# Kernel tuning notes

Measured on AMD Instinct MI355X. Metric: run time of the kernel, lower is better.

## Reference

```python
import jax, jax.numpy as jnp
import numpy as np

B, S, D, H = 2, 2048, 1024, 16
DK = D // H  # 64


def setup_inputs() -> dict:
    key = jax.random.key(0)
    ks = jax.random.split(key, 9)
    w = lambda k_, shp: jax.random.normal(k_, shp, dtype=jnp.float32) * 0.02
    inp = {
        "q": jax.random.normal(ks[0], (B, S, D), dtype=jnp.float32),
        "k": jax.random.normal(ks[1], (B, S, D), dtype=jnp.float32),
        "v": jax.random.normal(ks[2], (B, S, D), dtype=jnp.float32),
        # causal mask, broadcastable over [B, H, S, S]; 0 -> masked
        "mask": jnp.tril(jnp.ones((S, S), dtype=jnp.int32))[None, None, :, :],
        "Wq": w(ks[3], (D, D)), "bq": w(ks[4], (D,)),
        "Wk": w(ks[5], (D, D)), "bk": w(ks[6], (D,)),
        "Wv": w(ks[7], (D, D)), "bv": w(ks[8], (D,)),
    }
    return inp


def _head_split(x):
    # [B, S, D] -> [B, H, S, DK]
    return x.reshape(B, S, H, DK).transpose(0, 2, 1, 3)


def reference(q, k, v, mask, Wq, bq, Wk, bk, Wv, bv):
    qh = _head_split(q @ Wq + bq)
    kh = _head_split(k @ Wk + bk)
    vh = _head_split(v @ Wv + bv)

    scores = jnp.einsum("bhqd,bhkd->bhqk", qh, kh) / jnp.sqrt(jnp.float32(DK))
    scores = jnp.where(mask == 0, -jnp.inf, scores)
    # original subtracts the GLOBAL max of the whole score tensor, then softmax
    scores = jax.nn.softmax(scores - jnp.max(scores), axis=-1)
    scores = jnp.where(jnp.isnan(scores), 0.0, scores)  # fully-masked rows -> 0

    out = jnp.einsum("bhqk,bhkd->bhqd", scores, vh)
    return out.transpose(0, 2, 1, 3).reshape(B, S, D)
```

## Files before the change

### kernel.cpp

```cpp
#include <hip/hip_runtime.h>
#include <hip/hip_bf16.h>
#include <stdint.h>

#define BB 2
#define SS 2048
#define DD 1024
#define HH 16
#define DKK 64

typedef __attribute__((ext_vector_type(8)))  __bf16 bfvec8;
typedef __attribute__((ext_vector_type(4)))  __bf16 bfvec4;
typedef __attribute__((ext_vector_type(4)))  float  f32x4;
typedef __attribute__((ext_vector_type(16))) float  f32x16;
typedef __attribute__((ext_vector_type(4)))  unsigned int u32x4;

__device__ __forceinline__ float exp2_fast(float x) {
    float r;
    asm("v_exp_f32 %0, %1" : "=v"(r) : "v"(x));
    return r;
}
__device__ __forceinline__ uint32_t cvt_pk(float lo, float hi) {
    uint32_t r;
    asm("v_cvt_pk_bf16_f32 %0, %1, %2" : "=v"(r) : "v"(lo), "v"(hi));
    return r;
}
__device__ __forceinline__ void plswap(uint32_t &x, uint32_t &y) {
    asm("v_permlane32_swap_b32 %0, %1" : "+v"(x), "+v"(y));
}
__device__ __forceinline__ f32x16 zero16() {
    return (f32x16){0.f,0.f,0.f,0.f,0.f,0.f,0.f,0.f,
                    0.f,0.f,0.f,0.f,0.f,0.f,0.f,0.f};
}
#define MFMA32(A, B, C) __builtin_amdgcn_mfma_f32_32x32x16_bf16((A), (B), (C), 0, 0, 0)

#define PACK(st, bofs, pa) do {                                   \
    uint32_t A1 = cvt_pk((st)[(bofs)+0], (st)[(bofs)+1]);         \
    uint32_t B1 = cvt_pk((st)[(bofs)+4], (st)[(bofs)+5]);         \
    uint32_t A2 = cvt_pk((st)[(bofs)+2], (st)[(bofs)+3]);         \
    uint32_t B2 = cvt_pk((st)[(bofs)+6], (st)[(bofs)+7]);         \
    plswap(A1, B1); plswap(A2, B2);                               \
    u32x4 u_; u_[0] = A1; u_[1] = A2; u_[2] = B1; u_[3] = B2;     \
    (pa) = __builtin_bit_cast(bfvec8, u_);                        \
} while (0)

__global__ void wt_kernel(const float* __restrict__ Wq, const float* __restrict__ Wk,
                          const float* __restrict__ Wv,
                          __bf16* __restrict__ Wtq, __bf16* __restrict__ Wtk,
                          __bf16* __restrict__ Wtv) {
    const float* W  = (blockIdx.z == 0) ? Wq  : (blockIdx.z == 1) ? Wk  : Wv;
    __bf16*      Wt = (blockIdx.z == 0) ? Wtq : (blockIdx.z == 1) ? Wtk : Wtv;
    __shared__ float tile[32][33];
    int k0 = blockIdx.x * 32;
    int n0 = blockIdx.y * 32;
    int tx = threadIdx.x, ty = threadIdx.y;
    for (int j = 0; j < 32; j += 8)
        tile[ty + j][tx] = W[(size_t)(k0 + ty + j) * DD + n0 + tx];
    __syncthreads();
    for (int j = 0; j < 32; j += 8)
        Wt[(size_t)(n0 + ty + j) * DD + k0 + tx] = (__bf16)tile[tx][ty + j];
}

#define BM 128
#define BN 128
#define BKP 64
#define LDA 72
#define LDV 68

__global__ __launch_bounds__(256)
void proj_kernel(const float* __restrict__ Xq, const float* __restrict__ Xk,
                 const float* __restrict__ Xv,
                 const __bf16* __restrict__ Wtq, const __bf16* __restrict__ Wtk,
                 const __bf16* __restrict__ Wtv,
                 const float* __restrict__ bq, const float* __restrict__ bk,
                 const float* __restrict__ bv,
                 __bf16* __restrict__ Qh, __bf16* __restrict__ Kh,
                 __bf16* __restrict__ VtG)
{
    int z = blockIdx.z;
    const float*  X    = (z == 0) ? Xq  : (z == 1) ? Xk  : Xv;
    const __bf16* Wt   = (z == 0) ? Wtq : (z == 1) ? Wtk : Wtv;
    const float*  bias = (z == 0) ? bq  : (z == 1) ? bk  : bv;
    const float scale  = (z == 0) ? 0.125f * 1.44269504088896340736f : 1.0f;

    __shared__ __align__(16) char praw[2 * BM * LDA * 2];
    __bf16* As = reinterpret_cast<__bf16*>(praw);
    __bf16* Bs = reinterpret_cast<__bf16*>(praw + BM * LDA * 2);

    int row_tile = blockIdx.x * 4 + (blockIdx.y >> 3);
    int col_tile = blockIdx.y & 7;
    int row0 = row_tile * BM;
    int col0 = col_tile * BN;

    int t    = threadIdx.x;
    int lane = t & 63;
    int w    = t >> 6;
    int wm   = w >> 1, wn = w & 1;
    int l15  = lane & 15;
    int hi   = lane >> 4;
    int kg   = hi * 8;

    f32x4 acc[4][4];
    for (int i = 0; i < 4; ++i)
        for (int j = 0; j < 4; ++j)
            acc[i][j] = (f32x4){0.f, 0.f, 0.f, 0.f};

    int rr = t >> 3;
    int c8 = (t & 7) * 8;

    f32x4 a0[4], a1[4];
    bfvec8 br[4];
    for (int i = 0; i < 4; ++i) {
        int row = rr + 32 * i;
        const float* xp = &X[(size_t)(row0 + row) * DD + c8];
        a0[i] = *reinterpret_cast<const f32x4*>(xp);
        a1[i] = *reinterpret_cast<const f32x4*>(xp + 4);
        br[i] = *reinterpret_cast<const bfvec8*>(
            &Wt[(size_t)(col0 + row) * DD + c8]);
    }

    #pragma unroll 2
    for (int k0 = 0; k0 < DD; k0 += BKP) {
        for (int i = 0; i < 4; ++i) {
            int row = rr + 32 * i;
            bfvec8 av;
            av[0] = (__bf16)a0[i][0]; av[1] = (__bf16)a0[i][1];
            av[2] = (__bf16)a0[i][2]; av[3] = (__bf16)a0[i][3];
            av[4] = (__bf16)a1[i][0]; av[5] = (__bf16)a1[i][1];
            av[6] = (__bf16)a1[i][2]; av[7] = (__bf16)a1[i][3];
            *reinterpret_cast<bfvec8*>(&As[row * LDA + c8]) = av;
            *reinterpret_cast<bfvec8*>(&Bs[row * LDA + c8]) = br[i];
        }
        __syncthreads();

        bool more = (k0 + BKP) < DD;
        if (more) {
            int kn = k0 + BKP;
            for (int i = 0; i < 4; ++i) {
                int row = rr + 32 * i;
                const float* xp = &X[(size_t)(row0 + row) * DD + kn + c8];
                a0[i] = *reinterpret_cast<const f32x4*>(xp);
                a1[i] = *reinterpret_cast<const f32x4*>(xp + 4);
                br[i] = *reinterpret_cast<const bfvec8*>(
                    &Wt[(size_t)(col0 + row) * DD + kn + c8]);
            }
        }

        __builtin_amdgcn_s_setprio(1);
        for (int kk = 0; kk < BKP; kk += 32) {
            bfvec8 af[4], bf[4];
            for (int fm = 0; fm < 4; ++fm)
                af[fm] = *reinterpret_cast<const bfvec8*>(
                    &As[(wm * 64 + fm * 16 + l15) * LDA + kk + kg]);
            for (int fn = 0; fn < 4; ++fn)
                bf[fn] = *reinterpret_cast<const bfvec8*>(
                    &Bs[(wn * 64 + fn * 16 + l15) * LDA + kk + kg]);
            for (int fm = 0; fm < 4; ++fm)
                for (int fn = 0; fn < 4; ++fn)
                    acc[fm][fn] = __builtin_amdgcn_mfma_f32_16x16x32_bf16(
                        af[fm], bf[fn], acc[fm][fn], 0, 0, 0);
        }
        __builtin_amdgcn_s_setprio(0);
        __syncthreads();
    }

    if (z != 2) {
        __bf16* Out = (z == 0) ? Qh : Kh;
        for (int fn = 0; fn < 4; ++fn) {
            int n  = col0 + wn * 64 + fn * 16 + l15;
            float bvl = bias[n];
            int h = n >> 6, dk = n & 63;
            for (int fm = 0; fm < 4; ++fm) {
                int mbase = row0 + wm * 64 + fm * 16 + hi * 4;
                for (int r = 0; r < 4; ++r) {
                    int m = mbase + r;
                    int b = m >> 11, s = m & 2047;
                    float v = (acc[fm][fn][r] + bvl) * scale;
                    Out[(((size_t)(b * HH + h) * SS) + s) * DKK + dk] = (__bf16)v;
                }
            }
        }
    } else {
        __bf16* tw = reinterpret_cast<__bf16*>(praw + w * (64 * LDV * 2));
        for (int fn = 0; fn < 4; ++fn) {
            int n  = col0 + wn * 64 + fn * 16 + l15;
            float bvl = bias[n];
            for (int fm = 0; fm < 4; ++fm) {
                int sl = fm * 16 + hi * 4;
                for (int r = 0; r < 4; ++r)
                    tw[(sl + r) * LDV + fn * 16 + l15] =
                        (__bf16)(acc[fm][fn][r] + bvl);
            }
        }
        int h  = (col0 + wn * 64) >> 6;
        int b  = row0 >> 11;
        int bh = b * HH + h;
        int sg = (row0 & 2047) + wm * 64;
        int d  = lane;
        __bf16* dst = VtG + ((size_t)bh * DKK + d) * SS + sg;
        for (int c = 0; c < 64; c += 8) {
            bfvec8 v;
            #pragma unroll
            for (int j = 0; j < 8; ++j)
                v[j] = tw[(c + j) * LDV + d];
            *reinterpret_cast<bfvec8*>(&dst[c]) = v;
        }
    }
}

#define QB 128
#define KB 64
#define LDK 72
#define NT (SS / QB)

__global__ __launch_bounds__(512, 4)
void attn_kernel(const __bf16* __restrict__ Qh, const __bf16* __restrict__ Kh,
                 const __bf16* __restrict__ VtG, float* __restrict__ out)
{
    __shared__ __align__(16) char ldsraw[36864 + 1024];
    __bf16* KsA = reinterpret_cast<__bf16*>(ldsraw);
    __bf16* KsB = reinterpret_cast<__bf16*>(ldsraw + 9216);
    __bf16* VsA = reinterpret_cast<__bf16*>(ldsraw + 18432);
    __bf16* VsB = reinterpret_cast<__bf16*>(ldsraw + 27648);
    float*  smc = reinterpret_cast<float*>(ldsraw + 36864);
    float*  mrg = reinterpret_cast<float*>(ldsraw);
    float*  ml  = reinterpret_cast<float*>(ldsraw + 32768);

    int bh = blockIdx.x;
    int qt = (NT - 1) - blockIdx.y;
    const size_t base = (size_t)bh * SS * DKK;
    const __bf16* Kb = Kh + base;
    const __bf16* Vb = VtG + base;

    int t    = threadIdx.x;
    int lane = t & 63;
    int w    = t >> 6;
    int rg   = w & 3;
    int half = w >> 2;
    int l31  = lane & 31;
    int hi2  = lane >> 5;

    int a    = qt * QB + rg * 32;
    int qrow = a + l31;

    const __bf16* ksb = half ? KsB : KsA;
    const __bf16* vsb = half ? VsB : VsA;

    bfvec8 qf0, qf1, qf2, qf3;
    {
        const __bf16* qp = &Qh[base + (size_t)qrow * DKK + hi2 * 8];
        qf0 = *reinterpret_cast<const bfvec8*>(qp);
        qf1 = *reinterpret_cast<const bfvec8*>(qp + 16);
        qf2 = *reinterpret_cast<const bfvec8*>(qp + 32);
        qf3 = *reinterpret_cast<const bfvec8*>(qp + 48);
    }

    f32x16 acc0 = zero16(), acc1 = zero16();
    float mrow = -1e30f, lrow = 0.f;

    int nkv   = (a + 31) / KB + 1;
    int pairs = qt + 1;

    int srow = t >> 3;
    int c8   = (t & 7) * 8;

    {
        bfvec8 ka = *reinterpret_cast<const bfvec8*>(&Kb[(size_t)srow * DKK + c8]);
        bfvec8 va = *reinterpret_cast<const bfvec8*>(&Vb[(size_t)srow * SS + c8]);
        bfvec8 kb = *reinterpret_cast<const bfvec8*>(&Kb[(size_t)(64 + srow) * DKK + c8]);
        bfvec8 vb = *reinterpret_cast<const bfvec8*>(&Vb[(size_t)srow * SS + 64 + c8]);
        *reinterpret_cast<bfvec8*>(&KsA[srow * LDK + c8]) = ka;
        *reinterpret_cast<bfvec8*>(&VsA[srow * LDK + c8]) = va;
        *reinterpret_cast<bfvec8*>(&KsB[srow * LDK + c8]) = kb;
        *reinterpret_cast<bfvec8*>(&VsB[srow * LDK + c8]) = vb;
    }
    __syncthreads();

    for (int j = 0; ; ++j) {
        bool more = (j + 1) < pairs;

        bfvec8 pkA, pvA, pkB, pvB;
        if (more) {
            int t0 = (2 * j + 2) * KB;
            pkA = *reinterpret_cast<const bfvec8*>(&Kb[(size_t)(t0 + srow) * DKK + c8]);
            pvA = *reinterpret_cast<const bfvec8*>(&Vb[(size_t)srow * SS + t0 + c8]);
            pkB = *reinterpret_cast<const bfvec8*>(&Kb[(size_t)(t0 + 64 + srow) * DKK + c8]);
            pvB = *reinterpret_cast<const bfvec8*>(&Vb[(size_t)srow * SS + t0 + 64 + c8]);
        }

        int tj = 2 * j + half;
        if (tj < nkv) {
            int kv64 = tj * KB;

            f32x16 st0 = zero16(), st1 = zero16();
            {
                int off = l31 * LDK + hi2 * 8;
                bfvec8 k0 = *reinterpret_cast<const bfvec8*>(&ksb[off]);
                bfvec8 k1 = *reinterpret_cast<const bfvec8*>(&ksb[off + 16]);
                bfvec8 k2 = *reinterpret_cast<const bfvec8*>(&ksb[off + 32]);
                bfvec8 k3 = *reinterpret_cast<const bfvec8*>(&ksb[off + 48]);
                st0 = MFMA32(k0, qf0, st0); st0 = MFMA32(k1, qf1, st0);
                st0 = MFMA32(k2, qf2, st0); st0 = MFMA32(k3, qf3, st0);
                int off1 = off + 32 * LDK;
                bfvec8 m0 = *reinterpret_cast<const bfvec8*>(&ksb[off1]);
                bfvec8 m1 = *reinterpret_cast<const bfvec8*>(&ksb[off1 + 16]);
                bfvec8 m2v = *reinterpret_cast<const bfvec8*>(&ksb[off1 + 32]);
                bfvec8 m3 = *reinterpret_cast<const bfvec8*>(&ksb[off1 + 48]);
                st1 = MFMA32(m0, qf0, st1); st1 = MFMA32(m1, qf1, st1);
                st1 = MFMA32(m2v, qf2, st1); st1 = MFMA32(m3, qf3, st1);
            }

            if (kv64 + 63 > a) {
                #pragma unroll
                for (int r = 0; r < 16; ++r) {
                    int cr = ((r & 3) + 8 * (r >> 2)) + 4 * hi2;
                    st0[r] = (kv64 + cr      > qrow) ? -1e30f : st0[r];
                    st1[r] = (kv64 + 32 + cr > qrow) ? -1e30f : st1[r];
                }
            }

            float m2 = -1e30f;
            #pragma unroll
            for (int r = 0; r < 16; ++r) {
                m2 = fmaxf(m2, st0[r]);
                m2 = fmaxf(m2, st1[r]);
            }
            m2 = fmaxf(m2, __shfl_xor(m2, 32));

            float corr = 1.0f;
            if (!__all(m2 - mrow <= 8.0f)) {
                float mn = fmaxf(mrow, m2);
                corr = exp2_fast(mrow - mn);
                mrow = mn;
                smc[w * 32 + l31] = corr;
                #pragma unroll
                for (int r = 0; r < 16; ++r) {
                    float rc = smc[w * 32 + ((r & 3) + 8 * (r >> 2)) + 4 * hi2];
                    acc0[r] *= rc;
                    acc1[r] *= rc;
                }
            }

            float rs = 0.f;
            #pragma unroll
            for (int r = 0; r < 16; ++r) {
                float p0 = exp2_fast(st0[r] - mrow); st0[r] = p0;
                float p1 = exp2_fast(st1[r] - mrow); st1[r] = p1;
                rs += p0 + p1;
            }
            rs += __shfl_xor(rs, 32);
            lrow = lrow * corr + rs;

            bfvec8 pa0, pa1, pa2, pa3;
            PACK(st0, 0, pa0); PACK(st0, 8, pa1);
            PACK(st1, 0, pa2); PACK(st1, 8, pa3);

            {
                int voff = l31 * LDK + hi2 * 8;
                bfvec8 v0 = *reinterpret_cast<const bfvec8*>(&vsb[voff]);
                bfvec8 v1 = *reinterpret_cast<const bfvec8*>(&vsb[voff + 16]);
                bfvec8 v2 = *reinterpret_cast<const bfvec8*>(&vsb[voff + 32]);
                bfvec8 v3 = *reinterpret_cast<const bfvec8*>(&vsb[voff + 48]);
                acc0 = MFMA32(pa0, v0, acc0); acc0 = MFMA32(pa1, v1, acc0);
                acc0 = MFMA32(pa2, v2, acc0); acc0 = MFMA32(pa3, v3, acc0);
                int voff1 = voff + 32 * LDK;
                bfvec8 u0 = *reinterpret_cast<const bfvec8*>(&vsb[voff1]);
                bfvec8 u1 = *reinterpret_cast<const bfvec8*>(&vsb[voff1 + 16]);
                bfvec8 u2 = *reinterpret_cast<const bfvec8*>(&vsb[voff1 + 32]);
                bfvec8 u3 = *reinterpret_cast<const bfvec8*>(&vsb[voff1 + 48]);
                acc1 = MFMA32(pa0, u0, acc1); acc1 = MFMA32(pa1, u1, acc1);
                acc1 = MFMA32(pa2, u2, acc1); acc1 = MFMA32(pa3, u3, acc1);
            }
        }

        if (!more) break;
        __syncthreads();
        *reinterpret_cast<bfvec8*>(&KsA[srow * LDK + c8]) = pkA;
        *reinterpret_cast<bfvec8*>(&VsA[srow * LDK + c8]) = pvA;
        *reinterpret_cast<bfvec8*>(&KsB[srow * LDK + c8]) = pkB;
        *reinterpret_cast<bfvec8*>(&VsB[srow * LDK + c8]) = pvB;
        __syncthreads();
    }

    __syncthreads();
    if (half == 1) {
        float* dst = mrg + ((size_t)(rg * 64 + lane)) * 32;
        #pragma unroll
        for (int r = 0; r < 16; ++r) { dst[r] = acc0[r]; dst[16 + r] = acc1[r]; }
        if (hi2 == 0) {
            ml[rg * 32 + l31]       = mrow;
            ml[128 + rg * 32 + l31] = lrow;
        }
    }
    __syncthreads();
    if (half == 0) {
        float mU = ml[rg * 32 + l31];
        float lU = ml[128 + rg * 32 + l31];
        float mS = fmaxf(mrow, mU);
        float cL = exp2_fast(mrow - mS), cU = exp2_fast(mU - mS);
        float li = 1.0f / (lrow * cL + lU * cU);
        smc[rg * 32 + l31]       = cL * li;
        smc[(rg + 4) * 32 + l31] = cU * li;
        const float* src = mrg + ((size_t)(rg * 64 + lane)) * 32;
        int b = bh >> 4, h = bh & 15;
        #pragma unroll
        for (int r = 0; r < 16; ++r) {
            int cr = ((r & 3) + 8 * (r >> 2)) + 4 * hi2;
            float sA = smc[rg * 32 + cr];
            float sB = smc[(rg + 4) * 32 + cr];
            int sg = a + cr;
            size_t o = ((size_t)(b * SS + sg)) * DD + h * DKK + l31;
            out[o]      = acc0[r] * sA + src[r]      * sB;
            out[o + 32] = acc1[r] * sA + src[16 + r] * sB;
        }
    }
}

extern "C" void kernel_launch(void* const* d_in, const int* in_sizes, int n_in,
                              void* d_out, int out_size, void* d_ws, size_t ws_size,
                              hipStream_t stream)
{
    const float* q  = (const float*)d_in[0];
    const float* k  = (const float*)d_in[1];
    const float* v  = (const float*)d_in[2];
    const float* Wq = (const float*)d_in[4];
    const float* bq = (const float*)d_in[5];
    const float* Wk = (const float*)d_in[6];
    const float* bk = (const float*)d_in[7];
    const float* Wv = (const float*)d_in[8];
    const float* bv = (const float*)d_in[9];
    float* out = (float*)d_out;

    char* ws = (char*)d_ws;
    __bf16* Qh  = (__bf16*)(ws + (size_t)0);
    __bf16* Kh  = (__bf16*)(ws + (size_t)8  * 1024 * 1024);
    __bf16* VtG = (__bf16*)(ws + (size_t)24 * 1024 * 1024);
    __bf16* Wtq = (__bf16*)(ws + (size_t)32 * 1024 * 1024);
    __bf16* Wtk = (__bf16*)(ws + (size_t)34 * 1024 * 1024);
    __bf16* Wtv = (__bf16*)(ws + (size_t)36 * 1024 * 1024);

    wt_kernel<<<dim3(32, 32, 3), dim3(32, 8), 0, stream>>>(
        Wq, Wk, Wv, Wtq, Wtk, Wtv);

    proj_kernel<<<dim3(8, 32, 3), 256, 0, stream>>>(
        q, k, v, Wtq, Wtk, Wtv, bq, bk, bv, Qh, Kh, VtG);

    attn_kernel<<<dim3(32, NT), 512, 0, stream>>>(Qh, Kh, VtG, out);
}
```

Measured before the change: 96.55 us.

## Pre-convert activations to bf16 and stage projection tiles with global_load_lds

Adds a separate kernel that converts the fp32 q/k/v activations to bf16, using the output buffer and a workspace slot as scratch. The projection GEMM then loads bf16 tiles straight into LDS through global_load_lds, which removes the register prefetch and in-register conversion. It also drops the LDS row padding, so the MFMA fragment reads may hit bank conflicts. The register double-buffer prefetch is gone, so global loads are no longer overlapped with compute, and the extra kernel adds a full read and write pass over the activations.

```diff
diff --git a/kernel.cpp b/kernel.cpp
--- a/kernel.cpp
+++ b/kernel.cpp
@@ -13,6 +13,13 @@
 typedef __attribute__((ext_vector_type(4)))  float  f32x4;
 typedef __attribute__((ext_vector_type(16))) float  f32x16;
 typedef __attribute__((ext_vector_type(4)))  unsigned int u32x4;
+
+typedef __attribute__((address_space(1))) const unsigned int gas_uint;
+typedef __attribute__((address_space(3))) unsigned int las_uint;
+
+__device__ __forceinline__ void gload16(const void* g, void* l) {
+    __builtin_amdgcn_global_load_lds((gas_uint*)g, (las_uint*)l, 16, 0, 0);
+}
 
 __device__ __forceinline__ float exp2_fast(float x) {
     float r;
@@ -42,6 +49,23 @@
     u32x4 u_; u_[0] = A1; u_[1] = A2; u_[2] = B1; u_[3] = B2;     \
     (pa) = __builtin_bit_cast(bfvec8, u_);                        \
 } while (0)
+
+__global__ void xcvt_kernel(const float* __restrict__ q, const float* __restrict__ k,
+                            const float* __restrict__ v,
+                            __bf16* __restrict__ xq, __bf16* __restrict__ xk,
+                            __bf16* __restrict__ xv) {
+    const float* src = (blockIdx.z == 0) ? q  : (blockIdx.z == 1) ? k  : v;
+    __bf16*      dst = (blockIdx.z == 0) ? xq : (blockIdx.z == 1) ? xk : xv;
+    size_t i = ((size_t)blockIdx.x * 256 + threadIdx.x) * 8;
+    f32x4 a = *reinterpret_cast<const f32x4*>(&src[i]);
+    f32x4 b = *reinterpret_cast<const f32x4*>(&src[i + 4]);
+    bfvec8 o;
+    o[0] = (__bf16)a[0]; o[1] = (__bf16)a[1];
+    o[2] = (__bf16)a[2]; o[3] = (__bf16)a[3];
+    o[4] = (__bf16)b[0]; o[5] = (__bf16)b[1];
+    o[6] = (__bf16)b[2]; o[7] = (__bf16)b[3];
+    *reinterpret_cast<bfvec8*>(&dst[i]) = o;
+}
 
 __global__ void wt_kernel(const float* __restrict__ Wq, const float* __restrict__ Wk,
                           const float* __restrict__ Wv,
@@ -63,12 +87,11 @@
 #define BM 128
 #define BN 128
 #define BKP 64
-#define LDA 72
 #define LDV 68
 
 __global__ __launch_bounds__(256)
-void proj_kernel(const float* __restrict__ Xq, const float* __restrict__ Xk,
-                 const float* __restrict__ Xv,
+void proj_kernel(const __bf16* __restrict__ Xq, const __bf16* __restrict__ Xk,
+                 const __bf16* __restrict__ Xv,
                  const __bf16* __restrict__ Wtq, const __bf16* __restrict__ Wtk,
                  const __bf16* __restrict__ Wtv,
                  const float* __restrict__ bq, const float* __restrict__ bk,
@@ -77,14 +100,14 @@
                  __bf16* __restrict__ VtG)
 {
     int z = blockIdx.z;
-    const float*  X    = (z == 0) ? Xq  : (z == 1) ? Xk  : Xv;
+    const __bf16* X    = (z == 0) ? Xq  : (z == 1) ? Xk  : Xv;
     const __bf16* Wt   = (z == 0) ? Wtq : (z == 1) ? Wtk : Wtv;
     const float*  bias = (z == 0) ? bq  : (z == 1) ? bk  : bv;
     const float scale  = (z == 0) ? 0.125f * 1.44269504088896340736f : 1.0f;
 
-    __shared__ __align__(16) char praw[2 * BM * LDA * 2];
+    __shared__ __align__(16) char praw[36864];
     __bf16* As = reinterpret_cast<__bf16*>(praw);
-    __bf16* Bs = reinterpret_cast<__bf16*>(praw + BM * LDA * 2);
+    __bf16* Bs = reinterpret_cast<__bf16*>(praw + 16384);
 
     int row_tile = blockIdx.x * 4 + (blockIdx.y >> 3);
     int col_tile = blockIdx.y & 7;
@@ -104,56 +127,28 @@
         for (int j = 0; j < 4; ++j)
             acc[i][j] = (f32x4){0.f, 0.f, 0.f, 0.f};
 
-    int rr = t >> 3;
-    int c8 = (t & 7) * 8;
-
-    f32x4 a0[4], a1[4];
-    bfvec8 br[4];
-    for (int i = 0; i < 4; ++i) {
-        int row = rr + 32 * i;
-        const float* xp = &X[(size_t)(row0 + row) * DD + c8];
-        a0[i] = *reinterpret_cast<const f32x4*>(xp);
-        a1[i] = *reinterpret_cast<const f32x4*>(xp + 4);
-        br[i] = *reinterpret_cast<const bfvec8*>(
-            &Wt[(size_t)(col0 + row) * DD + c8]);
-    }
+    int gr = lane >> 3;
+    int gc = (lane & 7) * 8;
 
     #pragma unroll 2
     for (int k0 = 0; k0 < DD; k0 += BKP) {
+        #pragma unroll
         for (int i = 0; i < 4; ++i) {
-            int row = rr + 32 * i;
-            bfvec8 av;
-            av[0] = (__bf16)a0[i][0]; av[1] = (__bf16)a0[i][1];
-            av[2] = (__bf16)a0[i][2]; av[3] = (__bf16)a0[i][3];
-            av[4] = (__bf16)a1[i][0]; av[5] = (__bf16)a1[i][1];
-            av[6] = (__bf16)a1[i][2]; av[7] = (__bf16)a1[i][3];
-            *reinterpret_cast<bfvec8*>(&As[row * LDA + c8]) = av;
-            *reinterpret_cast<bfvec8*>(&Bs[row * LDA + c8]) = br[i];
+            int r = w * 32 + i * 8;
+            gload16(&X [(size_t)(row0 + r + gr) * DD + k0 + gc], &As[r * BKP]);
+            gload16(&Wt[(size_t)(col0 + r + gr) * DD + k0 + gc], &Bs[r * BKP]);
         }
         __syncthreads();
-
-        bool more = (k0 + BKP) < DD;
-        if (more) {
-            int kn = k0 + BKP;
-            for (int i = 0; i < 4; ++i) {
-                int row = rr + 32 * i;
-                const float* xp = &X[(size_t)(row0 + row) * DD + kn + c8];
-                a0[i] = *reinterpret_cast<const f32x4*>(xp);
-                a1[i] = *reinterpret_cast<const f32x4*>(xp + 4);
-                br[i] = *reinterpret_cast<const bfvec8*>(
-                    &Wt[(size_t)(col0 + row) * DD + kn + c8]);
-            }
-        }
 
         __builtin_amdgcn_s_setprio(1);
         for (int kk = 0; kk < BKP; kk += 32) {
             bfvec8 af[4], bf[4];
             for (int fm = 0; fm < 4; ++fm)
                 af[fm] = *reinterpret_cast<const bfvec8*>(
-                    &As[(wm * 64 + fm * 16 + l15) * LDA + kk + kg]);
+                    &As[(wm * 64 + fm * 16 + l15) * BKP + kk + kg]);
             for (int fn = 0; fn < 4; ++fn)
                 bf[fn] = *reinterpret_cast<const bfvec8*>(
-                    &Bs[(wn * 64 + fn * 16 + l15) * LDA + kk + kg]);
+                    &Bs[(wn * 64 + fn * 16 + l15) * BKP + kk + kg]);
             for (int fm = 0; fm < 4; ++fm)
                 for (int fn = 0; fn < 4; ++fn)
                     acc[fm][fn] = __builtin_amdgcn_mfma_f32_16x16x32_bf16(
@@ -180,7 +175,7 @@
             }
         }
     } else {
-        __bf16* tw = reinterpret_cast<__bf16*>(praw + w * (64 * LDV * 2));
+        __bf16* tw = reinterpret_cast<__bf16*>(praw) + w * (64 * LDV);
         for (int fn = 0; fn < 4; ++fn) {
             int n  = col0 + wn * 64 + fn * 16 + l15;
             float bvl = bias[n];
@@ -433,16 +428,22 @@
     char* ws = (char*)d_ws;
     __bf16* Qh  = (__bf16*)(ws + (size_t)0);
     __bf16* Kh  = (__bf16*)(ws + (size_t)8  * 1024 * 1024);
+    __bf16* Xbv = (__bf16*)(ws + (size_t)16 * 1024 * 1024);
     __bf16* VtG = (__bf16*)(ws + (size_t)24 * 1024 * 1024);
     __bf16* Wtq = (__bf16*)(ws + (size_t)32 * 1024 * 1024);
     __bf16* Wtk = (__bf16*)(ws + (size_t)34 * 1024 * 1024);
     __bf16* Wtv = (__bf16*)(ws + (size_t)36 * 1024 * 1024);
+    __bf16* Xbq = (__bf16*)d_out;
+    __bf16* Xbk = (__bf16*)d_out + (size_t)BB * SS * DD;
+
+    xcvt_kernel<<<dim3(BB * SS * DD / 2048, 1, 3), 256, 0, stream>>>(
+        q, k, v, Xbq, Xbk, Xbv);
 
     wt_kernel<<<dim3(32, 32, 3), dim3(32, 8), 0, stream>>>(
         Wq, Wk, Wv, Wtq, Wtk, Wtv);
 
     proj_kernel<<<dim3(8, 32, 3), 256, 0, stream>>>(
-        q, k, v, Wtq, Wtk, Wtv, bq, bk, bv, Qh, Kh, VtG);
+        Xbq, Xbk, Xbv, Wtq, Wtk, Wtv, bq, bk, bv, Qh, Kh, VtG);
 
     attn_kernel<<<dim3(32, NT), 512, 0, stream>>>(Qh, Kh, VtG, out);
 }
```

Result: slower. 114.0 us (+18.0%).
